# Kernel tuning notes

Measured on AMD Instinct MI355X. Metric: run time of the kernel, lower is better.

## Reference

```python
import jax, jax.numpy as jnp
import numpy as np

DIM = 2048
ORDER = 1
# upper-triangular index pairs (i<j), row-major over i then j — matches torch loop order
_IU_ROWS, _IU_COLS = np.triu_indices(DIM, k=1)


def setup_inputs() -> dict:
    key = jax.random.key(0)
    k1, k2 = jax.random.split(key)
    num_params = DIM * (DIM - 1) // 2
    x = jax.random.normal(k1, (4, 4096, DIM), dtype=jnp.float32)
    angles = jax.random.normal(k2, (num_params,), dtype=jnp.float32) * 0.01
    bias = jnp.zeros((DIM,), dtype=jnp.float32)
    return {"x": x, "angles": angles, "bias": bias}


def _skew_symmetric(angles):
    # A[i,j] = angles[k], A[j,i] = -angles[k] for upper-tri (i<j)
    A = jnp.zeros((DIM, DIM), dtype=angles.dtype)
    A = A.at[_IU_ROWS, _IU_COLS].set(angles)
    return A - A.T


def _cayley_approx(A, order=ORDER):
    # W = (I + A + ... + A^order) @ (I + A)
    I = jnp.eye(DIM, dtype=A.dtype)
    inv_approx = I
    A_power = A
    for _ in range(order):
        inv_approx = inv_approx + A_power
        A_power = A_power @ A
    return inv_approx @ (I + A)


def reference(x, angles, bias):
    A = _skew_symmetric(angles)
    W = _cayley_approx(A)
    # [b, s, d] @ [d, d] -> [b, s, d]
    out = jnp.einsum('bsd,de->bse', x, W) + bias
    return out
```

## Files before the change

kernel.cpp:

```cpp
#include <hip/hip_runtime.h>
#include <stdint.h>

#define DIM 2048

typedef short short8 __attribute__((ext_vector_type(8)));
typedef float f32x4 __attribute__((ext_vector_type(4)));

__device__ __forceinline__ unsigned short f2bf(float f) {
    union { float f; unsigned int u; } v;
    v.f = f;
    unsigned int r = v.u + 0x7FFFu + ((v.u >> 16) & 1u);
    return (unsigned short)(r >> 16);
}
__device__ __forceinline__ float bf2f(unsigned short u) {
    union { unsigned int u; float f; } v;
    v.u = ((unsigned int)u) << 16;
    return v.f;
}

__device__ __forceinline__ void async16(const unsigned short* g, unsigned short* l) {
    __builtin_amdgcn_global_load_lds(
        (__attribute__((address_space(1))) void*)(uintptr_t)g,
        (__attribute__((address_space(3))) void*)(uintptr_t)l,
        16, 0, 0);
}

__global__ __launch_bounds__(256) void build_A_tiled(const float* __restrict__ ang,
                                                     unsigned short* __restrict__ A) {
    __shared__ float tile[64][65];
    int b = blockIdx.x;
    int ti = 0, rem = b;
    while (rem >= 32 - ti) { rem -= 32 - ti; ++ti; }
    const int tj = ti + rem;
    const int t  = threadIdx.x;
    const int lj = t & 63;
    const int lw = t >> 6;
    const bool diag = (ti == tj);

#pragma unroll
    for (int m = 0; m < 16; ++m) {
        const int li = lw * 16 + m;
        const int i = ti * 64 + li;
        const int j = tj * 64 + lj;
        float v = 0.0f;
        if (i < j) v = ang[i * (4095 - i) / 2 + (j - i - 1)];
        tile[li][lj] = v;
    }
    __syncthreads();

#pragma unroll
    for (int m = 0; m < 16; ++m) {
        const int li = lw * 16 + m;
        float v;
        if (diag) {
            if (li < lj)      v =  tile[li][lj];
            else if (li > lj) v = -tile[lj][li];
            else              v = 0.0f;
        } else {
            v = tile[li][lj];
        }
        A[(size_t)(ti * 64 + li) * DIM + tj * 64 + lj] = f2bf(v);
    }
    if (!diag) {
#pragma unroll
        for (int m = 0; m < 16; ++m) {
            const int li = lw * 16 + m;
            A[(size_t)(tj * 64 + li) * DIM + ti * 64 + lj] = f2bf(-tile[lj][li]);
        }
    }
}

__global__ void cvt_f32_bf16(const float* __restrict__ in, unsigned short* __restrict__ out) {
    int i = (blockIdx.x * 256 + threadIdx.x) * 4;
    const float4 v = *(const float4*)(in + i);
    ushort4 o;
    o.x = f2bf(v.x); o.y = f2bf(v.y); o.z = f2bf(v.z); o.w = f2bf(v.w);
    *(ushort4*)(out + i) = o;
}

__global__ __launch_bounds__(256) void gemm_s64(
        const unsigned short* __restrict__ A,
        unsigned short* __restrict__ Wt) {
    __shared__ __align__(16) unsigned short ldsA[64 * 64];
    __shared__ __align__(16) unsigned short ldsB[64 * 64];
    const int K = DIM, N = DIM;

    const int t    = threadIdx.x;
    const int bn   = blockIdx.x * 64;
    const int bm   = blockIdx.y * 64;
    const int lane = t & 63;
    const int wave = t >> 6;
    const int waveM = (wave >> 1) * 32;
    const int waveN = (wave & 1) * 32;
    const int fm = lane & 15;
    const int fq = lane >> 4;

    f32x4 acc[2][2];
#pragma unroll
    for (int i = 0; i < 2; ++i)
#pragma unroll
        for (int j = 0; j < 2; ++j)
            acc[i][j] = (f32x4){0.f, 0.f, 0.f, 0.f};

    const int trow   = t >> 3;
    const int tchunk = (t & 7) ^ (trow & 7);
    const unsigned short* gA = A + (size_t)(bm + trow) * K + tchunk * 8;
    const unsigned short* gB = A + (size_t)(bn + trow) * K + tchunk * 8;
    const size_t rowskip = (size_t)32 * K;
    unsigned short* lA = ldsA + t * 8;
    unsigned short* lB = ldsB + t * 8;

    for (int kt = 0; kt < K; kt += 64) {
        __syncthreads();
        async16(gA + kt, lA);
        async16(gA + kt + rowskip, lA + 2048);
        async16(gB + kt, lB);
        async16(gB + kt + rowskip, lB + 2048);
        __syncthreads();

#pragma unroll
        for (int ks = 0; ks < 2; ++ks) {
            short8 af[2], bfv[2];
#pragma unroll
            for (int i = 0; i < 2; ++i) {
                const int rowA = waveM + i * 16 + fm;
                const int rowB = waveN + i * 16 + fm;
                af[i]  = *(const short8*)(ldsA + rowA * 64 + (((ks << 2) + fq) ^ (rowA & 7)) * 8);
                bfv[i] = *(const short8*)(ldsB + rowB * 64 + (((ks << 2) + fq) ^ (rowB & 7)) * 8);
            }
#pragma unroll
            for (int i = 0; i < 2; ++i)
#pragma unroll
                for (int j = 0; j < 2; ++j)
                    acc[i][j] = __builtin_amdgcn_mfma_f32_16x16x32_bf16(
                        af[i], bfv[j], acc[i][j], 0, 0, 0);
        }
    }

#pragma unroll
    for (int i = 0; i < 2; ++i) {
#pragma unroll
        for (int j = 0; j < 2; ++j) {
            const int col = bn + waveN + j * 16 + fm;
#pragma unroll
            for (int r = 0; r < 4; ++r) {
                const int row = bm + waveM + i * 16 + fq * 4 + r;
                const float a = bf2f(A[(size_t)row * N + col]);
                const float w = (row == col ? 1.0f : 0.0f) - 2.0f * a - acc[i][j][r];
                Wt[(size_t)row * N + col] = f2bf(w);
            }
        }
    }
}

__global__ __launch_bounds__(256) void gemm_main(
        const unsigned short* __restrict__ Aop,
        const unsigned short* __restrict__ Bop,
        int M, int N, int K,
        const float* __restrict__ bias,
        float* __restrict__ out) {
    __shared__ __align__(16) unsigned short ldsA[128 * 64];
    __shared__ __align__(16) unsigned short ldsB[128 * 64];

    const int t    = threadIdx.x;
    const int bn   = blockIdx.x * 128;
    const int bm   = blockIdx.y * 128;
    const int lane = t & 63;
    const int wave = t >> 6;
    const int waveM = (wave >> 1) * 64;
    const int waveN = (wave & 1) * 64;
    const int fm = lane & 15;
    const int fq = lane >> 4;

    f32x4 acc[4][4];
#pragma unroll
    for (int i = 0; i < 4; ++i)
#pragma unroll
        for (int j = 0; j < 4; ++j)
            acc[i][j] = (f32x4){0.f, 0.f, 0.f, 0.f};

    const int trow   = t >> 3;
    const int tchunk = (t & 7) ^ (trow & 7);
    const unsigned short* gA = Aop + (size_t)(bm + trow) * K + tchunk * 8;
    const unsigned short* gB = Bop + (size_t)(bn + trow) * K + tchunk * 8;
    const size_t rowskip = (size_t)32 * K;
    unsigned short* lA = ldsA + t * 8;
    unsigned short* lB = ldsB + t * 8;

    for (int kt = 0; kt < K; kt += 64) {
        __syncthreads();
#pragma unroll
        for (int i = 0; i < 4; ++i) {
            async16(gA + kt + i * rowskip, lA + i * 2048);
            async16(gB + kt + i * rowskip, lB + i * 2048);
        }
        __syncthreads();

#pragma unroll
        for (int ks = 0; ks < 2; ++ks) {
            short8 af[4], bfv[4];
#pragma unroll
            for (int i = 0; i < 4; ++i) {
                const int rowA = waveM + i * 16 + fm;
                const int rowB = waveN + i * 16 + fm;
                af[i]  = *(const short8*)(ldsA + rowA * 64 + (((ks << 2) + fq) ^ (rowA & 7)) * 8);
                bfv[i] = *(const short8*)(ldsB + rowB * 64 + (((ks << 2) + fq) ^ (rowB & 7)) * 8);
            }
#pragma unroll
            for (int i = 0; i < 4; ++i)
#pragma unroll
                for (int j = 0; j < 4; ++j)
                    acc[i][j] = __builtin_amdgcn_mfma_f32_16x16x32_bf16(
                        af[i], bfv[j], acc[i][j], 0, 0, 0);
        }
    }

#pragma unroll
    for (int i = 0; i < 4; ++i) {
#pragma unroll
        for (int j = 0; j < 4; ++j) {
            const int col = bn + waveN + j * 16 + fm;
#pragma unroll
            for (int r = 0; r < 4; ++r) {
                const int row = bm + waveM + i * 16 + fq * 4 + r;
                out[(size_t)row * N + col] = acc[i][j][r] + bias[col];
            }
        }
    }
}

extern "C" void kernel_launch(void* const* d_in, const int* in_sizes, int n_in,
                              void* d_out, int out_size, void* d_ws, size_t ws_size,
                              hipStream_t stream) {
    const float* x      = (const float*)d_in[0];
    const float* angles = (const float*)d_in[1];
    const float* bias   = (const float*)d_in[2];
    float* out = (float*)d_out;

    char* ws = (char*)d_ws;
    unsigned short* Abf = (unsigned short*)ws;
    unsigned short* Wt  = (unsigned short*)(ws + (8u << 20));
    unsigned short* xbf = (unsigned short*)(ws + (16u << 20));

    const int M = 4 * 4096;
    const int n_elem_x = M * DIM;

    build_A_tiled<<<528, 256, 0, stream>>>(angles, Abf);
    cvt_f32_bf16<<<(n_elem_x / 4) / 256, 256, 0, stream>>>(x, xbf);

    gemm_s64<<<dim3(DIM / 64, DIM / 64), 256, 0, stream>>>(Abf, Wt);

    gemm_main<<<dim3(DIM / 128, M / 128), 256, 0, stream>>>(
        xbf, Wt, M, DIM, DIM, bias, out);
}
```

Measured before the change: 406.2 us.

## Rewrite main GEMM as 256x256 double-buffered 8-wave pipelined kernel

The main x@W GEMM moves from a 128x128 tile with 4 waves and single-buffered LDS to a 256x256 tile with 8 waves and two LDS buffers. Global-to-LDS async loads for the next K tile are interleaved between MFMA quadrants, with explicit vmcnt waits, barriers and s_setprio around the MFMA bursts. The goal is to hide load latency and raise reuse per byte loaded, at the cost of 128KB of LDS per block, heavier register pressure and fewer blocks in flight.

```diff
diff --git a/kernel.cpp b/kernel.cpp
--- a/kernel.cpp
+++ b/kernel.cpp
@@ -153,78 +153,127 @@
     }
 }
 
-__global__ __launch_bounds__(256) void gemm_main(
+
+#define WAITV(N) asm volatile("s_waitcnt vmcnt(" #N ")" ::: "memory")
+#define BAR() do { asm volatile("" ::: "memory"); __builtin_amdgcn_s_barrier(); asm volatile("" ::: "memory"); } while (0)
+
+#define STG_A(BUF, R0, KT) async16(gA + (size_t)(R0) * 2048 + (KT), &ldsA[BUF][(R0) * 64 + t * 8])
+#define STG_B(BUF, R0, KT) async16(gB + (size_t)(R0) * 2048 + (KT), &ldsB[BUF][(R0) * 64 + t * 8])
+
+#define READ_A(BUF, IH) do { \
+    _Pragma("unroll") \
+    for (int ii = 0; ii < 4; ++ii) { \
+        const int row  = waveM + (IH) * 64 + ii * 16 + fm; \
+        const int base = row * 64; \
+        af[ii][0] = *(const short8*)(&ldsA[BUF][base + ((fq    ) ^ (row & 7)) * 8]); \
+        af[ii][1] = *(const short8*)(&ldsA[BUF][base + ((fq + 4) ^ (row & 7)) * 8]); \
+    } } while (0)
+
+#define READ_B(BUF, JH) do { \
+    _Pragma("unroll") \
+    for (int jj = 0; jj < 2; ++jj) { \
+        const int row  = (JH) * 128 + wn * 32 + jj * 16 + fm; \
+        const int base = row * 64; \
+        bfr[JH][jj][0] = *(const short8*)(&ldsB[BUF][base + ((fq    ) ^ (row & 7)) * 8]); \
+        bfr[JH][jj][1] = *(const short8*)(&ldsB[BUF][base + ((fq + 4) ^ (row & 7)) * 8]); \
+    } } while (0)
+
+#define MMAQ(IH, JH) do { \
+    __builtin_amdgcn_s_setprio(1); \
+    _Pragma("unroll") \
+    for (int ks = 0; ks < 2; ++ks) \
+    _Pragma("unroll") \
+    for (int ii = 0; ii < 4; ++ii) \
+    _Pragma("unroll") \
+    for (int jj = 0; jj < 2; ++jj) \
+        acc[(IH) * 4 + ii][(JH) * 2 + jj] = __builtin_amdgcn_mfma_f32_16x16x32_bf16( \
+            af[ii][ks], bfr[JH][jj][ks], acc[(IH) * 4 + ii][(JH) * 2 + jj], 0, 0, 0); \
+    __builtin_amdgcn_s_setprio(0); \
+} while (0)
+
+#define KTILE(BUF, KTN, PRE, VN) do { \
+    WAITV(VN); \
+    BAR(); \
+     \
+    READ_A(BUF, 0); \
+    READ_B(BUF, 0); \
+    MMAQ(0, 0); \
+    BAR(); \
+     \
+    if (PRE) { STG_A(BUF, 0, KTN); STG_A(BUF, 128, KTN); } \
+    READ_B(BUF, 1); \
+    MMAQ(0, 1); \
+    BAR(); \
+     \
+    if (PRE) { STG_B(BUF, 0, KTN); STG_B(BUF, 64, KTN); } \
+    READ_A(BUF, 1); \
+    MMAQ(1, 0); \
+    BAR(); \
+     \
+    if (PRE) { STG_B(BUF, 128, KTN); STG_B(BUF, 192, KTN); STG_A(BUF, 64, KTN); STG_A(BUF, 192, KTN); } \
+    MMAQ(1, 1); \
+    BAR(); \
+} while (0)
+
+__global__ __launch_bounds__(512, 2) void gemm_main(
         const unsigned short* __restrict__ Aop,
         const unsigned short* __restrict__ Bop,
         int M, int N, int K,
         const float* __restrict__ bias,
         float* __restrict__ out) {
-    __shared__ __align__(16) unsigned short ldsA[128 * 64];
-    __shared__ __align__(16) unsigned short ldsB[128 * 64];
+    __shared__ __align__(16) unsigned short ldsA[2][256 * 64];
+    __shared__ __align__(16) unsigned short ldsB[2][256 * 64];
 
     const int t    = threadIdx.x;
-    const int bn   = blockIdx.x * 128;
-    const int bm   = blockIdx.y * 128;
+    const int bn   = blockIdx.x * 256;
+    const int bm   = blockIdx.y * 256;
     const int lane = t & 63;
     const int wave = t >> 6;
-    const int waveM = (wave >> 1) * 64;
-    const int waveN = (wave & 1) * 64;
+    const int wm   = wave >> 2;
+    const int wn   = wave & 3;
+    const int waveM = wm * 128;
     const int fm = lane & 15;
     const int fq = lane >> 4;
 
-    f32x4 acc[4][4];
-#pragma unroll
-    for (int i = 0; i < 4; ++i)
+    f32x4 acc[8][4];
+#pragma unroll
+    for (int i = 0; i < 8; ++i)
 #pragma unroll
         for (int j = 0; j < 4; ++j)
             acc[i][j] = (f32x4){0.f, 0.f, 0.f, 0.f};
 
+    short8 af[4][2];
+    short8 bfr[2][2][2];
+
     const int trow   = t >> 3;
     const int tchunk = (t & 7) ^ (trow & 7);
-    const unsigned short* gA = Aop + (size_t)(bm + trow) * K + tchunk * 8;
-    const unsigned short* gB = Bop + (size_t)(bn + trow) * K + tchunk * 8;
-    const size_t rowskip = (size_t)32 * K;
-    unsigned short* lA = ldsA + t * 8;
-    unsigned short* lB = ldsB + t * 8;
-
-    for (int kt = 0; kt < K; kt += 64) {
-        __syncthreads();
-#pragma unroll
-        for (int i = 0; i < 4; ++i) {
-            async16(gA + kt + i * rowskip, lA + i * 2048);
-            async16(gB + kt + i * rowskip, lB + i * 2048);
-        }
-        __syncthreads();
-
-#pragma unroll
-        for (int ks = 0; ks < 2; ++ks) {
-            short8 af[4], bfv[4];
-#pragma unroll
-            for (int i = 0; i < 4; ++i) {
-                const int rowA = waveM + i * 16 + fm;
-                const int rowB = waveN + i * 16 + fm;
-                af[i]  = *(const short8*)(ldsA + rowA * 64 + (((ks << 2) + fq) ^ (rowA & 7)) * 8);
-                bfv[i] = *(const short8*)(ldsB + rowB * 64 + (((ks << 2) + fq) ^ (rowB & 7)) * 8);
-            }
-#pragma unroll
-            for (int i = 0; i < 4; ++i)
-#pragma unroll
-                for (int j = 0; j < 4; ++j)
-                    acc[i][j] = __builtin_amdgcn_mfma_f32_16x16x32_bf16(
-                        af[i], bfv[j], acc[i][j], 0, 0, 0);
-        }
-    }
-
-#pragma unroll
-    for (int i = 0; i < 4; ++i) {
+    const unsigned short* gA = Aop + (size_t)(bm + trow) * 2048 + tchunk * 8;
+    const unsigned short* gB = Bop + (size_t)(bn + trow) * 2048 + tchunk * 8;
+
+    STG_A(0, 0, 0);   STG_A(0, 128, 0);  STG_B(0, 0, 0);   STG_B(0, 64, 0);
+    STG_B(0, 128, 0); STG_B(0, 192, 0);  STG_A(0, 64, 0);  STG_A(0, 192, 0);
+    STG_A(1, 0, 64);  STG_A(1, 128, 64); STG_B(1, 0, 64);  STG_B(1, 64, 64);
+    STG_B(1, 128, 64);STG_B(1, 192, 64); STG_A(1, 64, 64); STG_A(1, 192, 64);
+
+#pragma unroll 1
+    for (int it = 0; it < 15; ++it) {
+        const int kt = it * 128;
+        KTILE(0, kt + 128, true, 8);
+        KTILE(1, kt + 192, true, 8);
+    }
+    KTILE(0, 0, false, 8);
+    KTILE(1, 0, false, 0);
+
+#pragma unroll
+    for (int i = 0; i < 8; ++i) {
+        const int row0 = bm + waveM + i * 16 + fq * 4;
 #pragma unroll
         for (int j = 0; j < 4; ++j) {
-            const int col = bn + waveN + j * 16 + fm;
-#pragma unroll
-            for (int r = 0; r < 4; ++r) {
-                const int row = bm + waveM + i * 16 + fq * 4 + r;
-                out[(size_t)row * N + col] = acc[i][j][r] + bias[col];
-            }
+            const int col = bn + (j >> 1) * 128 + wn * 32 + (j & 1) * 16 + fm;
+            const float b = bias[col];
+#pragma unroll
+            for (int r = 0; r < 4; ++r)
+                out[(size_t)(row0 + r) * 2048 + col] = acc[i][j][r] + b;
         }
     }
 }
@@ -250,6 +299,6 @@
 
     gemm_s64<<<dim3(DIM / 64, DIM / 64), 256, 0, stream>>>(Abf, Wt);
 
-    gemm_main<<<dim3(DIM / 128, M / 128), 256, 0, stream>>>(
+    gemm_main<<<dim3(DIM / 256, M / 256), 512, 0, stream>>>(
         xbf, Wt, M, DIM, DIM, bias, out);
 }
```

New measurement: 376.8 us. -7.2%, faster.
